# Kernel tuning notes

Hardware: AMD Instinct MI355X
Metric: run time of the kernel (lower is better)

## Reference

```python
import jax, jax.numpy as jnp
import numpy as np

B, T, V, E, U = 8192, 1, 4000, 256, 256
IN = E + E  # GRU input dim: concat(features[B,1,256], embedded tokens[B,1,256]) -> 512


def setup_inputs() -> dict:
    key = jax.random.key(0)
    ks = jax.random.split(key, 8)
    s = 0.05
    return {
        "tokens": jax.random.randint(ks[0], (B, T), 0, V),
        "features": jax.random.normal(ks[1], (B, E), jnp.float32),
        "hidden": jnp.zeros((B, U), jnp.float32),  # unused by the original call (gru gets no initial_state)
        "emb": jax.random.normal(ks[2], (V, E), jnp.float32) * s,
        "gru_kernel": jax.random.normal(ks[3], (IN, 3 * U), jnp.float32) * s,
        "gru_rkernel": jax.random.normal(ks[4], (U, 3 * U), jnp.float32) * s,
        "gru_bias": jnp.zeros((2, 3 * U), jnp.float32),  # reset_after=True: separate input/recurrent biases
        "fc1_w": jax.random.normal(ks[5], (U, U), jnp.float32) * s,
        "fc1_b": jnp.zeros((U,), jnp.float32),
        "fc2_w": jax.random.normal(ks[6], (U, V), jnp.float32) * s,
        "fc2_b": jnp.zeros((V,), jnp.float32),
    }


def reference(tokens, features, hidden, emb, gru_kernel, gru_rkernel, gru_bias,
              fc1_w, fc1_b, fc2_w, fc2_b):
    # Embedding lookup: [B,T,E]
    x = emb[tokens]
    # concat context vector on feature axis (forces T==1): [B,1,E+E]
    x = jnp.concatenate([features[:, None, :], x], axis=-1)
    # Keras GRU called without initial_state -> zeros initial state.
    h0 = jnp.zeros((x.shape[0], U), x.dtype)

    def step(h, xt):  # xt: [B, IN]; Keras GRU v3 (reset_after=True) cell; dropout off at inference
        gx = xt @ gru_kernel + gru_bias[0]      # [B, 3U]
        gh = h @ gru_rkernel + gru_bias[1]      # [B, 3U]
        xz, xr, xn = jnp.split(gx, 3, axis=-1)
        hz, hr, hn = jnp.split(gh, 3, axis=-1)
        z = jax.nn.sigmoid(xz + hz)
        r = jax.nn.sigmoid(xr + hr)
        n = jnp.tanh(xn + r * hn)
        h_new = z * h + (1.0 - z) * n
        return h_new, h_new

    state, seq = jax.lax.scan(step, h0, jnp.swapaxes(x, 0, 1))  # seq: [T,B,U]
    out = jnp.swapaxes(seq, 0, 1)               # [B,T,U]
    y = out @ fc1_w + fc1_b                     # [B,T,U]
    y = y.reshape(-1, y.shape[-1])              # [B*T, U]
    logits = y @ fc2_w + fc2_b                  # [B*T, V]
    return (logits, state)
```

## Files before the change

kernel.cpp:

```cpp
#include <hip/hip_runtime.h>
#include <stdint.h>

typedef unsigned short u16;
typedef __attribute__((ext_vector_type(8))) short bf16x8;
typedef __attribute__((ext_vector_type(4))) float f32x4;

#define Bsz   8192
#define Vv    4000
#define Ee    256
#define Uu    256
#define INd   512
#define G3    768

__device__ __forceinline__ u16 f2bf(float f) {
    union { float f; uint32_t i; } v; v.f = f;
    uint32_t x = v.i;
    return (u16)((x + 0x7fffu + ((x >> 16) & 1u)) >> 16);
}

__global__ __launch_bounds__(256) void gather_x(
    const int* __restrict__ tokens, const float* __restrict__ features,
    const float* __restrict__ emb, u16* __restrict__ x)
{
    int id = blockIdx.x * 256 + threadIdx.x;
    int b = id >> 6;
    int k = (id & 63) * 8;
    const float* src = (k < Ee) ? (features + (size_t)b * Ee + k)
                                : (emb + (size_t)tokens[b] * Ee + (k - Ee));
    float4 a = *(const float4*)src;
    float4 c = *(const float4*)(src + 4);
    u16 o[8] = {f2bf(a.x), f2bf(a.y), f2bf(a.z), f2bf(a.w),
                f2bf(c.x), f2bf(c.y), f2bf(c.z), f2bf(c.w)};
    *(uint4*)(x + (size_t)b * INd + k) = *(uint4*)o;
}

__global__ __launch_bounds__(256) void transpose_cvt(
    const float* __restrict__ in, u16* __restrict__ out, int logK, int N)
{
    int id = blockIdx.x * 256 + threadIdx.x;
    int n = id >> logK;
    int k = id & ((1 << logK) - 1);
    out[id] = f2bf(in[(size_t)k * N + n]);
}

#define BM 64
#define BN 64
#define BK 32
#define LDP 56

__global__ __launch_bounds__(256) void gemm_gru(
    const u16* __restrict__ A,
    const u16* __restrict__ BT,
    const float* __restrict__ gb,
    u16* __restrict__ h,
    float* __restrict__ state)
{
    __shared__ u16 As[BM][LDP];
    __shared__ u16 Bs[3][BN][LDP];

    int tid  = threadIdx.x;
    int m0   = blockIdx.y * BM;
    int n0   = blockIdx.x * BN;
    int wid  = tid >> 6;
    int lane = tid & 63;
    int quad = lane >> 4;
    int l16  = lane & 15;
    int wm   = (wid >> 1) * 32;
    int wn   = (wid & 1) * 32;

    f32x4 acc[3][2][2] = {};

    int ldr = tid >> 2;
    int ldc = (tid & 3) * 8;

    const u16* Arow = A + (size_t)(m0 + ldr) * INd + ldc;
    const u16* B0 = BT + (size_t)(n0 + ldr) * INd + ldc;
    const u16* B1 = BT + (size_t)(Uu + n0 + ldr) * INd + ldc;
    const u16* B2 = BT + (size_t)(2 * Uu + n0 + ldr) * INd + ldc;

    for (int k0 = 0; k0 < INd; k0 += BK) {
        __syncthreads();
        *(uint4*)&As[ldr][ldc]    = *(const uint4*)(Arow + k0);
        *(uint4*)&Bs[0][ldr][ldc] = *(const uint4*)(B0 + k0);
        *(uint4*)&Bs[1][ldr][ldc] = *(const uint4*)(B1 + k0);
        *(uint4*)&Bs[2][ldr][ldc] = *(const uint4*)(B2 + k0);
        __syncthreads();

        bf16x8 af0 = *(const bf16x8*)&As[wm + l16][quad * 8];
        bf16x8 af1 = *(const bf16x8*)&As[wm + 16 + l16][quad * 8];
        #pragma unroll
        for (int g = 0; g < 3; g++) {
            bf16x8 bf0 = *(const bf16x8*)&Bs[g][wn + l16][quad * 8];
            bf16x8 bf1 = *(const bf16x8*)&Bs[g][wn + 16 + l16][quad * 8];
            acc[g][0][0] = __builtin_amdgcn_mfma_f32_16x16x32_bf16(af0, bf0, acc[g][0][0], 0, 0, 0);
            acc[g][0][1] = __builtin_amdgcn_mfma_f32_16x16x32_bf16(af0, bf1, acc[g][0][1], 0, 0, 0);
            acc[g][1][0] = __builtin_amdgcn_mfma_f32_16x16x32_bf16(af1, bf0, acc[g][1][0], 0, 0, 0);
            acc[g][1][1] = __builtin_amdgcn_mfma_f32_16x16x32_bf16(af1, bf1, acc[g][1][1], 0, 0, 0);
        }
    }

    #pragma unroll
    for (int mi = 0; mi < 2; mi++)
    #pragma unroll
    for (int ni = 0; ni < 2; ni++) {
        int j = n0 + wn + ni * 16 + l16;
        float bz = gb[j]          + gb[G3 + j];
        float br = gb[Uu + j]     + gb[G3 + Uu + j];
        float b0n = gb[2 * Uu + j];
        float b1n = gb[G3 + 2 * Uu + j];
        #pragma unroll
        for (int r = 0; r < 4; r++) {
            int b = m0 + wm + mi * 16 + quad * 4 + r;
            float z  = 1.f / (1.f + __expf(-(acc[0][mi][ni][r] + bz)));
            float rr = 1.f / (1.f + __expf(-(acc[1][mi][ni][r] + br)));
            float n  = tanhf(acc[2][mi][ni][r] + b0n + rr * b1n);
            float hv = (1.f - z) * n;
            h[(size_t)b * Uu + j] = f2bf(hv);
            state[(size_t)b * Uu + j] = hv;
        }
    }
}

template<bool OUT_BF16>
__global__ __launch_bounds__(256) void gemm_bias(
    const u16* __restrict__ A, const u16* __restrict__ BT,
    const float* __restrict__ bias, void* __restrict__ Cout,
    int M, int N, int K)
{
    __shared__ u16 As[BM][LDP];
    __shared__ u16 Bs[BN][LDP];

    int tid  = threadIdx.x;
    int m0   = blockIdx.y * BM;
    int n0   = blockIdx.x * BN;
    int wid  = tid >> 6;
    int lane = tid & 63;
    int quad = lane >> 4;
    int l16  = lane & 15;
    int wm   = (wid >> 1) * 32;
    int wn   = (wid & 1) * 32;

    f32x4 acc[2][2] = {};

    int ldr = tid >> 2;
    int ldc = (tid & 3) * 8;

    const u16* Arow = A + (size_t)(m0 + ldr) * K + ldc;
    int nB = n0 + ldr;
    const u16* Brow = BT + (size_t)nB * K + ldc;
    bool bvalid = nB < N;

    for (int k0 = 0; k0 < K; k0 += BK) {
        __syncthreads();
        *(uint4*)&As[ldr][ldc] = *(const uint4*)(Arow + k0);
        uint4 bv = bvalid ? *(const uint4*)(Brow + k0) : make_uint4(0u, 0u, 0u, 0u);
        *(uint4*)&Bs[ldr][ldc] = bv;
        __syncthreads();

        bf16x8 af0 = *(const bf16x8*)&As[wm + l16][quad * 8];
        bf16x8 af1 = *(const bf16x8*)&As[wm + 16 + l16][quad * 8];
        bf16x8 bf0 = *(const bf16x8*)&Bs[wn + l16][quad * 8];
        bf16x8 bf1 = *(const bf16x8*)&Bs[wn + 16 + l16][quad * 8];

        acc[0][0] = __builtin_amdgcn_mfma_f32_16x16x32_bf16(af0, bf0, acc[0][0], 0, 0, 0);
        acc[0][1] = __builtin_amdgcn_mfma_f32_16x16x32_bf16(af0, bf1, acc[0][1], 0, 0, 0);
        acc[1][0] = __builtin_amdgcn_mfma_f32_16x16x32_bf16(af1, bf0, acc[1][0], 0, 0, 0);
        acc[1][1] = __builtin_amdgcn_mfma_f32_16x16x32_bf16(af1, bf1, acc[1][1], 0, 0, 0);
    }

    #pragma unroll
    for (int mi = 0; mi < 2; mi++)
    #pragma unroll
    for (int ni = 0; ni < 2; ni++) {
        int gn = n0 + wn + ni * 16 + l16;
        if (gn >= N) continue;
        float bvv = bias[gn];
        #pragma unroll
        for (int r = 0; r < 4; r++) {
            int gm = m0 + wm + mi * 16 + quad * 4 + r;
            float v = acc[mi][ni][r] + bvv;
            if (OUT_BF16) ((u16*)Cout)[(size_t)gm * N + gn] = f2bf(v);
            else          ((float*)Cout)[(size_t)gm * N + gn] = v;
        }
    }
}

extern "C" void kernel_launch(void* const* d_in, const int* in_sizes, int n_in,
                              void* d_out, int out_size, void* d_ws, size_t ws_size,
                              hipStream_t stream)
{
    const int*   tokens   = (const int*)d_in[0];
    const float* features = (const float*)d_in[1];
    const float* emb      = (const float*)d_in[3];
    const float* w1       = (const float*)d_in[4];
    const float* gbias    = (const float*)d_in[6];
    const float* fc1w     = (const float*)d_in[7];
    const float* fc1b     = (const float*)d_in[8];
    const float* fc2w     = (const float*)d_in[9];
    const float* fc2b     = (const float*)d_in[10];

    float* logits = (float*)d_out;
    float* state  = logits + (size_t)Bsz * Vv;

    char* ws = (char*)d_ws;
    u16* x    = (u16*)(ws);
    u16* w1t  = (u16*)(ws +  8388608);
    u16* fc1t = (u16*)(ws +  9175040);
    u16* fc2t = (u16*)(ws +  9306112);
    u16* h    = (u16*)(ws + 11354112);
    u16* y    = (u16*)(ws + 15548416);

    gather_x     <<<dim3(Bsz * 64 / 256), 256, 0, stream>>>(tokens, features, emb, x);
    transpose_cvt<<<dim3(G3 * INd / 256), 256, 0, stream>>>(w1,   w1t,  9, G3);
    transpose_cvt<<<dim3(Uu * Uu / 256),  256, 0, stream>>>(fc1w, fc1t, 8, Uu);
    transpose_cvt<<<dim3(Vv * Uu / 256),  256, 0, stream>>>(fc2w, fc2t, 8, Vv);

    gemm_gru<<<dim3(Uu / BN, Bsz / BM), 256, 0, stream>>>(x, w1t, gbias, h, state);

    gemm_bias<true><<<dim3(Uu / BN, Bsz / BM), 256, 0, stream>>>(
        h, fc1t, fc1b, (void*)y, Bsz, Uu, Uu);

    gemm_bias<false><<<dim3((Vv + BN - 1) / BN, Bsz / BM), 256, 0, stream>>>(
        y, fc2t, fc2b, (void*)logits, Bsz, Vv, Uu);
}
```

Baseline: 241.0 us.

## Use 128-wide GEMM tiles with direct-to-LDS loads and a fused tiled weight transpose

```diff
diff --git a/kernel.cpp b/kernel.cpp
--- a/kernel.cpp
+++ b/kernel.cpp
@@ -7,6 +7,7 @@
 
 #define Bsz   8192
 #define Vv    4000
+#define Vpad  4096
 #define Ee    256
 #define Uu    256
 #define INd   512
@@ -16,6 +17,12 @@
     union { float f; uint32_t i; } v; v.f = f;
     uint32_t x = v.i;
     return (u16)((x + 0x7fffu + ((x >> 16) & 1u)) >> 16);
+}
+
+__device__ __forceinline__ void gload16(const u16* g, u16* l) {
+    __builtin_amdgcn_global_load_lds(
+        (const __attribute__((address_space(1))) unsigned int*)g,
+        (__attribute__((address_space(3))) unsigned int*)l, 16, 0, 0);
 }
 
 __global__ __launch_bounds__(256) void gather_x(
@@ -34,19 +41,93 @@
     *(uint4*)(x + (size_t)b * INd + k) = *(uint4*)o;
 }
 
-__global__ __launch_bounds__(256) void transpose_cvt(
-    const float* __restrict__ in, u16* __restrict__ out, int logK, int N)
-{
-    int id = blockIdx.x * 256 + threadIdx.x;
-    int n = id >> logK;
-    int k = id & ((1 << logK) - 1);
-    out[id] = f2bf(in[(size_t)k * N + n]);
-}
-
-#define BM 64
-#define BN 64
-#define BK 32
-#define LDP 56
+__global__ __launch_bounds__(256) void transpose_all(
+    const float* __restrict__ w1,  u16* __restrict__ w1t,
+    const float* __restrict__ fc1, u16* __restrict__ fc1t,
+    const float* __restrict__ fc2, u16* __restrict__ fc2t)
+{
+    __shared__ float t[32][33];
+    int b = blockIdx.x;
+    const float* in; u16* out; int K, N, bx, by;
+    if (b < 384)      { in = w1;  out = w1t;  K = 512; N = 768;  bx = b % 24;  by = b / 24; }
+    else if (b < 448) { b -= 384; in = fc1; out = fc1t; K = 256; N = 256;  bx = b % 8;   by = b / 8; }
+    else              { b -= 448; in = fc2; out = fc2t; K = 256; N = Vv;   bx = b % 128; by = b / 128; }
+    int n0 = bx * 32, k0 = by * 32;
+    int c = threadIdx.x & 31, r = threadIdx.x >> 5;
+    int n = n0 + c;
+    #pragma unroll
+    for (int i = 0; i < 32; i += 8)
+        t[r + i][c] = (n < N) ? in[(size_t)(k0 + r + i) * N + n] : 0.f;
+    __syncthreads();
+    #pragma unroll
+    for (int i = 0; i < 32; i += 8)
+        out[(size_t)(n0 + r + i) * K + k0 + c] = f2bf(t[c][r + i]);
+}
+
+template<bool OUT_BF16>
+__global__ __launch_bounds__(256) void gemm128(
+    const u16* __restrict__ A, const u16* __restrict__ BT,
+    const float* __restrict__ bias, void* __restrict__ Cout,
+    int N, int K)
+{
+    __shared__ __align__(16) u16 As[128 * 32];
+    __shared__ __align__(16) u16 Bs[128 * 32];
+
+    int tid  = threadIdx.x;
+    int m0   = blockIdx.y * 128;
+    int n0   = blockIdx.x * 128;
+    int wid  = tid >> 6;
+    int lane = tid & 63;
+    int quad = lane >> 4;
+    int l16  = lane & 15;
+    int wm   = (wid >> 1) * 64;
+    int wn   = (wid & 1) * 64;
+
+    f32x4 acc[4][4] = {};
+
+    const u16* ag = A  + (size_t)(m0 + (tid >> 2)) * K + (tid & 3) * 8;
+    const u16* bg = BT + (size_t)(n0 + (tid >> 2)) * K + (tid & 3) * 8;
+    u16* lA = &As[tid * 8];
+    u16* lB = &Bs[tid * 8];
+
+    for (int k0 = 0; k0 < K; k0 += 32) {
+        __syncthreads();
+        gload16(ag + k0,            lA);
+        gload16(ag + 64 * K + k0,   lA + 64 * 32);
+        gload16(bg + k0,            lB);
+        gload16(bg + 64 * K + k0,   lB + 64 * 32);
+        __syncthreads();
+
+        bf16x8 af[4], bf[4];
+        #pragma unroll
+        for (int i = 0; i < 4; i++)
+            af[i] = *(const bf16x8*)&As[(wm + i * 16 + l16) * 32 + quad * 8];
+        #pragma unroll
+        for (int j = 0; j < 4; j++)
+            bf[j] = *(const bf16x8*)&Bs[(wn + j * 16 + l16) * 32 + quad * 8];
+        #pragma unroll
+        for (int i = 0; i < 4; i++)
+            #pragma unroll
+            for (int j = 0; j < 4; j++)
+                acc[i][j] = __builtin_amdgcn_mfma_f32_16x16x32_bf16(af[i], bf[j], acc[i][j], 0, 0, 0);
+    }
+
+    #pragma unroll
+    for (int i = 0; i < 4; i++)
+    #pragma unroll
+    for (int j = 0; j < 4; j++) {
+        int gn = n0 + wn + j * 16 + l16;
+        if (gn >= N) continue;
+        float bvv = bias[gn];
+        #pragma unroll
+        for (int r = 0; r < 4; r++) {
+            int gm = m0 + wm + i * 16 + quad * 4 + r;
+            float v = acc[i][j][r] + bvv;
+            if (OUT_BF16) ((u16*)Cout)[(size_t)gm * N + gn] = f2bf(v);
+            else          ((float*)Cout)[(size_t)gm * N + gn] = v;
+        }
+    }
+}
 
 __global__ __launch_bounds__(256) void gemm_gru(
     const u16* __restrict__ A,
@@ -55,132 +136,66 @@
     u16* __restrict__ h,
     float* __restrict__ state)
 {
-    __shared__ u16 As[BM][LDP];
-    __shared__ u16 Bs[3][BN][LDP];
+    __shared__ __align__(16) u16 As[128 * 32];
+    __shared__ __align__(16) u16 Bs[3][64 * 32];
 
     int tid  = threadIdx.x;
-    int m0   = blockIdx.y * BM;
-    int n0   = blockIdx.x * BN;
+    int m0   = blockIdx.y * 128;
+    int n0   = blockIdx.x * 64;
     int wid  = tid >> 6;
     int lane = tid & 63;
     int quad = lane >> 4;
     int l16  = lane & 15;
-    int wm   = (wid >> 1) * 32;
-    int wn   = (wid & 1) * 32;
-
-    f32x4 acc[3][2][2] = {};
-
-    int ldr = tid >> 2;
-    int ldc = (tid & 3) * 8;
-
-    const u16* Arow = A + (size_t)(m0 + ldr) * INd + ldc;
-    const u16* B0 = BT + (size_t)(n0 + ldr) * INd + ldc;
-    const u16* B1 = BT + (size_t)(Uu + n0 + ldr) * INd + ldc;
-    const u16* B2 = BT + (size_t)(2 * Uu + n0 + ldr) * INd + ldc;
-
-    for (int k0 = 0; k0 < INd; k0 += BK) {
-        __syncthreads();
-        *(uint4*)&As[ldr][ldc]    = *(const uint4*)(Arow + k0);
-        *(uint4*)&Bs[0][ldr][ldc] = *(const uint4*)(B0 + k0);
-        *(uint4*)&Bs[1][ldr][ldc] = *(const uint4*)(B1 + k0);
-        *(uint4*)&Bs[2][ldr][ldc] = *(const uint4*)(B2 + k0);
-        __syncthreads();
-
-        bf16x8 af0 = *(const bf16x8*)&As[wm + l16][quad * 8];
-        bf16x8 af1 = *(const bf16x8*)&As[wm + 16 + l16][quad * 8];
-        #pragma unroll
-        for (int g = 0; g < 3; g++) {
-            bf16x8 bf0 = *(const bf16x8*)&Bs[g][wn + l16][quad * 8];
-            bf16x8 bf1 = *(const bf16x8*)&Bs[g][wn + 16 + l16][quad * 8];
-            acc[g][0][0] = __builtin_amdgcn_mfma_f32_16x16x32_bf16(af0, bf0, acc[g][0][0], 0, 0, 0);
-            acc[g][0][1] = __builtin_amdgcn_mfma_f32_16x16x32_bf16(af0, bf1, acc[g][0][1], 0, 0, 0);
-            acc[g][1][0] = __builtin_amdgcn_mfma_f32_16x16x32_bf16(af1, bf0, acc[g][1][0], 0, 0, 0);
-            acc[g][1][1] = __builtin_amdgcn_mfma_f32_16x16x32_bf16(af1, bf1, acc[g][1][1], 0, 0, 0);
-        }
-    }
-
-    #pragma unroll
-    for (int mi = 0; mi < 2; mi++)
-    #pragma unroll
-    for (int ni = 0; ni < 2; ni++) {
-        int j = n0 + wn + ni * 16 + l16;
-        float bz = gb[j]          + gb[G3 + j];
-        float br = gb[Uu + j]     + gb[G3 + Uu + j];
-        float b0n = gb[2 * Uu + j];
-        float b1n = gb[G3 + 2 * Uu + j];
+    int wm   = wid * 32;
+
+    f32x4 acc[3][2][4] = {};
+
+    const u16* ag = A  + (size_t)(m0 + (tid >> 2)) * INd + (tid & 3) * 8;
+    const u16* bg = BT + (size_t)(n0 + (tid >> 2)) * INd + (tid & 3) * 8;
+    u16* lA = &As[tid * 8];
+    u16* lB = &Bs[0][tid * 8];
+
+    for (int k0 = 0; k0 < INd; k0 += 32) {
+        __syncthreads();
+        gload16(ag + k0,           lA);
+        gload16(ag + 64 * INd + k0, lA + 64 * 32);
+        #pragma unroll
+        for (int g = 0; g < 3; g++)
+            gload16(bg + (size_t)g * 256 * INd + k0, lB + g * 64 * 32);
+        __syncthreads();
+
+        bf16x8 af[2];
+        #pragma unroll
+        for (int i = 0; i < 2; i++)
+            af[i] = *(const bf16x8*)&As[(wm + i * 16 + l16) * 32 + quad * 8];
+        #pragma unroll
+        for (int g = 0; g < 3; g++)
+            #pragma unroll
+            for (int j = 0; j < 4; j++) {
+                bf16x8 bf = *(const bf16x8*)&Bs[g][(j * 16 + l16) * 32 + quad * 8];
+                acc[g][0][j] = __builtin_amdgcn_mfma_f32_16x16x32_bf16(af[0], bf, acc[g][0][j], 0, 0, 0);
+                acc[g][1][j] = __builtin_amdgcn_mfma_f32_16x16x32_bf16(af[1], bf, acc[g][1][j], 0, 0, 0);
+            }
+    }
+
+    #pragma unroll
+    for (int i = 0; i < 2; i++)
+    #pragma unroll
+    for (int j = 0; j < 4; j++) {
+        int jj = n0 + j * 16 + l16;
+        float bz  = gb[jj]          + gb[G3 + jj];
+        float br  = gb[Uu + jj]     + gb[G3 + Uu + jj];
+        float b0n = gb[2 * Uu + jj];
+        float b1n = gb[G3 + 2 * Uu + jj];
         #pragma unroll
         for (int r = 0; r < 4; r++) {
-            int b = m0 + wm + mi * 16 + quad * 4 + r;
-            float z  = 1.f / (1.f + __expf(-(acc[0][mi][ni][r] + bz)));
-            float rr = 1.f / (1.f + __expf(-(acc[1][mi][ni][r] + br)));
-            float n  = tanhf(acc[2][mi][ni][r] + b0n + rr * b1n);
+            int b = m0 + wm + i * 16 + quad * 4 + r;
+            float z  = 1.f / (1.f + __expf(-(acc[0][i][j][r] + bz)));
+            float rr = 1.f / (1.f + __expf(-(acc[1][i][j][r] + br)));
+            float n  = tanhf(acc[2][i][j][r] + b0n + rr * b1n);
             float hv = (1.f - z) * n;
-            h[(size_t)b * Uu + j] = f2bf(hv);
-            state[(size_t)b * Uu + j] = hv;
-        }
-    }
-}
-
-template<bool OUT_BF16>
-__global__ __launch_bounds__(256) void gemm_bias(
-    const u16* __restrict__ A, const u16* __restrict__ BT,
-    const float* __restrict__ bias, void* __restrict__ Cout,
-    int M, int N, int K)
-{
-    __shared__ u16 As[BM][LDP];
-    __shared__ u16 Bs[BN][LDP];
-
-    int tid  = threadIdx.x;
-    int m0   = blockIdx.y * BM;
-    int n0   = blockIdx.x * BN;
-    int wid  = tid >> 6;
-    int lane = tid & 63;
-    int quad = lane >> 4;
-    int l16  = lane & 15;
-    int wm   = (wid >> 1) * 32;
-    int wn   = (wid & 1) * 32;
-
-    f32x4 acc[2][2] = {};
-
-    int ldr = tid >> 2;
-    int ldc = (tid & 3) * 8;
-
-    const u16* Arow = A + (size_t)(m0 + ldr) * K + ldc;
-    int nB = n0 + ldr;
-    const u16* Brow = BT + (size_t)nB * K + ldc;
-    bool bvalid = nB < N;
-
-    for (int k0 = 0; k0 < K; k0 += BK) {
-        __syncthreads();
-        *(uint4*)&As[ldr][ldc] = *(const uint4*)(Arow + k0);
-        uint4 bv = bvalid ? *(const uint4*)(Brow + k0) : make_uint4(0u, 0u, 0u, 0u);
-        *(uint4*)&Bs[ldr][ldc] = bv;
-        __syncthreads();
-
-        bf16x8 af0 = *(const bf16x8*)&As[wm + l16][quad * 8];
-        bf16x8 af1 = *(const bf16x8*)&As[wm + 16 + l16][quad * 8];
-        bf16x8 bf0 = *(const bf16x8*)&Bs[wn + l16][quad * 8];
-        bf16x8 bf1 = *(const bf16x8*)&Bs[wn + 16 + l16][quad * 8];
-
-        acc[0][0] = __builtin_amdgcn_mfma_f32_16x16x32_bf16(af0, bf0, acc[0][0], 0, 0, 0);
-        acc[0][1] = __builtin_amdgcn_mfma_f32_16x16x32_bf16(af0, bf1, acc[0][1], 0, 0, 0);
-        acc[1][0] = __builtin_amdgcn_mfma_f32_16x16x32_bf16(af1, bf0, acc[1][0], 0, 0, 0);
-        acc[1][1] = __builtin_amdgcn_mfma_f32_16x16x32_bf16(af1, bf1, acc[1][1], 0, 0, 0);
-    }
-
-    #pragma unroll
-    for (int mi = 0; mi < 2; mi++)
-    #pragma unroll
-    for (int ni = 0; ni < 2; ni++) {
-        int gn = n0 + wn + ni * 16 + l16;
-        if (gn >= N) continue;
-        float bvv = bias[gn];
-        #pragma unroll
-        for (int r = 0; r < 4; r++) {
-            int gm = m0 + wm + mi * 16 + quad * 4 + r;
-            float v = acc[mi][ni][r] + bvv;
-            if (OUT_BF16) ((u16*)Cout)[(size_t)gm * N + gn] = f2bf(v);
-            else          ((float*)Cout)[(size_t)gm * N + gn] = v;
+            h[(size_t)b * Uu + jj] = f2bf(hv);
+            state[(size_t)b * Uu + jj] = hv;
         }
     }
 }
@@ -207,19 +222,17 @@
     u16* w1t  = (u16*)(ws +  8388608);
     u16* fc1t = (u16*)(ws +  9175040);
     u16* fc2t = (u16*)(ws +  9306112);
-    u16* h    = (u16*)(ws + 11354112);
-    u16* y    = (u16*)(ws + 15548416);
-
-    gather_x     <<<dim3(Bsz * 64 / 256), 256, 0, stream>>>(tokens, features, emb, x);
-    transpose_cvt<<<dim3(G3 * INd / 256), 256, 0, stream>>>(w1,   w1t,  9, G3);
-    transpose_cvt<<<dim3(Uu * Uu / 256),  256, 0, stream>>>(fc1w, fc1t, 8, Uu);
-    transpose_cvt<<<dim3(Vv * Uu / 256),  256, 0, stream>>>(fc2w, fc2t, 8, Vv);
-
-    gemm_gru<<<dim3(Uu / BN, Bsz / BM), 256, 0, stream>>>(x, w1t, gbias, h, state);
-
-    gemm_bias<true><<<dim3(Uu / BN, Bsz / BM), 256, 0, stream>>>(
-        h, fc1t, fc1b, (void*)y, Bsz, Uu, Uu);
-
-    gemm_bias<false><<<dim3((Vv + BN - 1) / BN, Bsz / BM), 256, 0, stream>>>(
-        y, fc2t, fc2b, (void*)logits, Bsz, Vv, Uu);
-}
+    u16* h    = (u16*)(ws + 11403264);
+    u16* y    = (u16*)(ws + 15597568);
+
+    gather_x<<<dim3(Bsz * 64 / 256), 256, 0, stream>>>(tokens, features, emb, x);
+    transpose_all<<<dim3(1472), 256, 0, stream>>>(w1, w1t, fc1w, fc1t, fc2w, fc2t);
+
+    gemm_gru<<<dim3(Uu / 64, Bsz / 128), 256, 0, stream>>>(x, w1t, gbias, h, state);
+
+    gemm128<true><<<dim3(Uu / 128, Bsz / 128), 256, 0, stream>>>(
+        h, fc1t, fc1b, (void*)y, Uu, Uu);
+
+    gemm128<false><<<dim3(Vpad / 128, Bsz / 128), 256, 0, stream>>>(
+        y, fc2t, fc2b, (void*)logits, Vv, Uu);
+}
```

Result: faster. 232.1 us (-3.7%).
